# Kernel optimization log

Measured on AMD Instinct MI355X. Metric: run time of the kernel, lower is better.

The kernel has to match this reference:

```python
import jax, jax.numpy as jnp
import numpy as np

B, T, QD, KD, AD = 64, 2048, 512, 512, 512
SCALING = 1.0
NEG = -1e10


def setup_inputs() -> dict:
    key = jax.random.key(0)
    ks = jax.random.split(key, 10)
    s = 0.02
    return {
        "query": jax.random.normal(ks[0], (B, QD), jnp.float32),
        "keys": jax.random.normal(ks[1], (B, T, KD), jnp.float32),
        "value": jax.random.normal(ks[2], (B, T, KD), jnp.float32),
        "cover": jax.random.uniform(ks[3], (B, T), jnp.float32),
        "key_len": jax.random.randint(ks[4], (B,), T // 2, T + 1),
        "Wq": jax.random.normal(ks[5], (QD, AD), jnp.float32) * s,
        "bq": jnp.zeros((AD,), jnp.float32),
        "Wk": jax.random.normal(ks[6], (KD, AD), jnp.float32) * s,
        "Wc": jax.random.normal(ks[7], (1, AD), jnp.float32) * s,
        "Wo": jax.random.normal(ks[8], (AD, 1), jnp.float32) * s,
    }


def reference(query, keys, value, cover, key_len, Wq, bq, Wk, Wc, Wo):
    # projections
    q = query @ Wq + bq                      # [B, A]
    k = jnp.einsum("btd,da->bta", keys, Wk)  # [B, T, A]
    c = cover[..., None] * Wc[0]             # [B, T, A]  (Linear(1, A), no bias)
    # additive energy
    e = jnp.tanh(q[:, None, :] + k + c)      # [B, T, A]
    energy = jnp.einsum("bta,ao->bot", e, Wo)  # [B, 1, T]
    # mask padded positions (t >= key_len)
    mask = jnp.arange(T)[None, None, :] >= key_len[:, None, None]  # [B, 1, T]
    energy = jnp.where(mask, NEG, energy)
    attn = jax.nn.softmax(energy * SCALING, axis=2)  # [B, 1, T]
    context = jnp.einsum("bqt,btd->bqd", attn, value)[:, 0, :]  # [B, KD]
    return context, attn
```

## Files before the change

kernel.cpp:

```cpp
#include <hip/hip_runtime.h>

#define B_ 64
#define T_ 2048
#define D_ 512
#define A_ 512
#define BM 128
#define BK 32
#define NSTEP (D_/BK)

typedef float f32x4_t __attribute__((ext_vector_type(4)));
typedef short bf16x8_t __attribute__((ext_vector_type(8)));

#define GLL16(g, l) __builtin_amdgcn_global_load_lds( \
    (const __attribute__((address_space(1))) void*)(g), \
    (__attribute__((address_space(3))) void*)(l), 16, 0, 0)

__device__ __forceinline__ unsigned int f2bf(float x) {
  union { float f; unsigned int u; } v; v.f = x;
  unsigned int r = ((v.u >> 16) & 1u) + 0x7FFFu;
  return (v.u + r) >> 16;
}
__device__ __forceinline__ unsigned int pack2(float lo, float hi) {
  return (f2bf(lo) & 0xFFFFu) | ((f2bf(hi) & 0xFFFFu) << 16);
}

__global__ void __launch_bounds__(256) qproj_kernel(
    const float* __restrict__ query, const float* __restrict__ Wq,
    const float* __restrict__ bq, float* __restrict__ qbuf) {
  __shared__ float qs[D_];
  const int b = blockIdx.x, tid = threadIdx.x;
  qs[tid] = query[b*D_ + tid];
  qs[tid+256] = query[b*D_ + tid + 256];
  __syncthreads();
  float a0 = bq[tid], a1 = bq[tid+256];
  for (int d = 0; d < D_; ++d) {
    const float qv = qs[d];
    a0 += qv * Wq[d*A_ + tid];
    a1 += qv * Wq[d*A_ + tid + 256];
  }
  qbuf[b*A_ + tid] = a0;
  qbuf[b*A_ + tid+256] = a1;
}

__global__ void __launch_bounds__(256) wkprep_kernel(
    const float* __restrict__ Wk, unsigned int* __restrict__ slab) {
  __shared__ float tile[32][65];
  const int kb = blockIdx.x >> 3;
  const int a0 = (blockIdx.x & 7) * 64;
  const int tid = threadIdx.x;
  for (int p = 0; p < 8; ++p) {
    const int idx = p*256 + tid;
    const int k = idx >> 6, al = idx & 63;
    tile[k][al] = Wk[(kb*32 + k)*A_ + a0 + al];
  }
  __syncthreads();
  const int al = tid >> 2, c = tid & 3;
  const int a = a0 + al;
  uint4 w;
  w.x = pack2(tile[c*8+0][al], tile[c*8+1][al]);
  w.y = pack2(tile[c*8+2][al], tile[c*8+3][al]);
  w.z = pack2(tile[c*8+4][al], tile[c*8+5][al]);
  w.w = pack2(tile[c*8+6][al], tile[c*8+7][al]);
  const int cpos = c ^ ((a >> 1) & 3);
  *(uint4*)(slab + (kb*512 + a)*16 + cpos*4) = w;
}

__global__ void __launch_bounds__(512) energy_kernel(
    const float* __restrict__ keys, const float* __restrict__ cover,
    const int* __restrict__ key_len, const unsigned char* __restrict__ slab,
    const float* __restrict__ qbuf, const float* __restrict__ Wc,
    const float* __restrict__ Wo, float* __restrict__ energy) {
  __shared__ __align__(16) unsigned char Abuf[2][BM*64];
  __shared__ __align__(16) unsigned char Bbuf[2][A_*64];
  __shared__ float redbuf[8][64];

  const int b = blockIdx.y;
  const int t0 = blockIdx.x * BM;
  const int kl = key_len[b];
  if (t0 >= kl) return;

  const int tid = threadIdx.x;
  const int wid = tid >> 6;
  const int lane = tid & 63;
  const int lq = lane >> 4, lr = lane & 15;
  const int wm = wid >> 2, wn = wid & 3;

  const int ar = tid >> 2, ac = tid & 3;
  const float* aptr = keys + ((size_t)b * T_ + t0 + ar) * D_ + ac * 8;
  const int a_dst = ar * 64 + ((ac ^ ((ar >> 1) & 3)) << 4);

  f32x4_t acc[4][8];
  #pragma unroll
  for (int i = 0; i < 4; ++i)
    #pragma unroll
    for (int j = 0; j < 8; ++j) acc[i][j] = 0.0f;

  int a_off[4], b_off[8];
  #pragma unroll
  for (int mf = 0; mf < 4; ++mf) {
    const int r = wm*64 + mf*16 + lr;
    a_off[mf] = r*64 + ((lq ^ ((r >> 1) & 3)) << 4);
  }
  #pragma unroll
  for (int nf = 0; nf < 8; ++nf) {
    const int r = wn*128 + nf*16 + lr;
    b_off[nf] = r*64 + ((lq ^ ((r >> 1) & 3)) << 4);
  }

  {
    const float4 v0 = *(const float4*)(aptr);
    const float4 v1 = *(const float4*)(aptr + 4);
    uint4 w;
    w.x = pack2(v0.x, v0.y); w.y = pack2(v0.z, v0.w);
    w.z = pack2(v1.x, v1.y); w.w = pack2(v1.z, v1.w);
    *(uint4*)(&Abuf[0][a_dst]) = w;
    const unsigned char* g = slab + wid*4096 + lane*16;
    unsigned char* l = &Bbuf[0][wid*4096];
    GLL16(g, l); GLL16(g+1024, l+1024); GLL16(g+2048, l+2048); GLL16(g+3072, l+3072);
  }
  __syncthreads();

  for (int ks = 0; ks < NSTEP; ++ks) {
    const int cur = ks & 1;
    const bool pre = (ks + 1 < NSTEP);
    float4 v0, v1;
    if (pre) {
      const float* p = aptr + (ks + 1) * BK;
      v0 = *(const float4*)(p);
      v1 = *(const float4*)(p + 4);
      const unsigned char* g = slab + (size_t)(ks+1)*32768 + wid*4096 + lane*16;
      unsigned char* l = &Bbuf[cur^1][wid*4096];
      GLL16(g, l); GLL16(g+1024, l+1024); GLL16(g+2048, l+2048); GLL16(g+3072, l+3072);
    }
    bf16x8_t aF[4], bF[8];
    #pragma unroll
    for (int mf = 0; mf < 4; ++mf) aF[mf] = *(const bf16x8_t*)(&Abuf[cur][a_off[mf]]);
    #pragma unroll
    for (int nf = 0; nf < 8; ++nf) bF[nf] = *(const bf16x8_t*)(&Bbuf[cur][b_off[nf]]);
    #pragma unroll
    for (int mf = 0; mf < 4; ++mf)
      #pragma unroll
      for (int nf = 0; nf < 8; ++nf)
        acc[mf][nf] = __builtin_amdgcn_mfma_f32_16x16x32_bf16(aF[mf], bF[nf], acc[mf][nf], 0, 0, 0);
    if (pre) {
      uint4 w;
      w.x = pack2(v0.x, v0.y); w.y = pack2(v0.z, v0.w);
      w.z = pack2(v1.x, v1.y); w.w = pack2(v1.z, v1.w);
      *(uint4*)(&Abuf[cur^1][a_dst]) = w;
    }
    __syncthreads();
  }

  float cov[4][4];
  #pragma unroll
  for (int mf = 0; mf < 4; ++mf)
    #pragma unroll
    for (int j = 0; j < 4; ++j)
      cov[mf][j] = cover[(size_t)b*T_ + t0 + wm*64 + mf*16 + lq*4 + j];

  float ep[4][4];
  #pragma unroll
  for (int mf = 0; mf < 4; ++mf)
    #pragma unroll
    for (int j = 0; j < 4; ++j) ep[mf][j] = 0.f;

  #pragma unroll
  for (int nf = 0; nf < 8; ++nf) {
    const int n = wn*128 + nf*16 + lr;
    const float qv = qbuf[b*A_ + n];
    const float wc = Wc[n];
    const float wo = Wo[n];
    #pragma unroll
    for (int mf = 0; mf < 4; ++mf)
      #pragma unroll
      for (int j = 0; j < 4; ++j) {
        float p = acc[mf][nf][j] + qv + cov[mf][j] * wc;
        p = fminf(fmaxf(p, -15.f), 15.f);
        const float t2 = __expf(2.f * p);
        ep[mf][j] += wo * ((t2 - 1.f) / (t2 + 1.f));
      }
  }
  #pragma unroll
  for (int mf = 0; mf < 4; ++mf)
    #pragma unroll
    for (int j = 0; j < 4; ++j) {
      float v = ep[mf][j];
      v += __shfl_xor(v, 1); v += __shfl_xor(v, 2);
      v += __shfl_xor(v, 4); v += __shfl_xor(v, 8);
      ep[mf][j] = v;
    }
  if (lr == 0) {
    #pragma unroll
    for (int mf = 0; mf < 4; ++mf)
      #pragma unroll
      for (int j = 0; j < 4; ++j)
        redbuf[wid][mf*16 + lq*4 + j] = ep[mf][j];
  }
  __syncthreads();
  if (tid < BM) {
    const int wmm = tid >> 6, rl = tid & 63;
    const float e = redbuf[wmm*4+0][rl] + redbuf[wmm*4+1][rl]
                  + redbuf[wmm*4+2][rl] + redbuf[wmm*4+3][rl];
    energy[b*T_ + t0 + tid] = e;
  }
}

__global__ void __launch_bounds__(1024) softmax_kernel(
    const float* __restrict__ energy, const int* __restrict__ key_len,
    float* __restrict__ attn) {
  __shared__ float sredM[16];
  __shared__ float sredS[16];
  const int b = blockIdx.x, tid = threadIdx.x;
  const int kl = key_len[b];
  const float e0 = (tid < kl) ? energy[b*T_ + tid] : -3.0e38f;
  const float e1 = (tid + 1024 < kl) ? energy[b*T_ + tid + 1024] : -3.0e38f;
  float m = fmaxf(e0, e1);
  for (int s = 32; s; s >>= 1) m = fmaxf(m, __shfl_xor(m, s));
  if ((tid & 63) == 0) sredM[tid >> 6] = m;
  __syncthreads();
  float M = -3.0e38f;
  #pragma unroll
  for (int i = 0; i < 16; ++i) M = fmaxf(M, sredM[i]);
  const float p0 = (tid < kl) ? __expf(e0 - M) : 0.f;
  const float p1 = (tid + 1024 < kl) ? __expf(e1 - M) : 0.f;
  float s = p0 + p1;
  for (int k = 32; k; k >>= 1) s += __shfl_xor(s, k);
  if ((tid & 63) == 0) sredS[tid >> 6] = s;
  __syncthreads();
  float S = 0.f;
  #pragma unroll
  for (int i = 0; i < 16; ++i) S += sredS[i];
  const float inv = 1.f / S;
  attn[b*T_ + tid] = p0 * inv;
  attn[b*T_ + tid + 1024] = p1 * inv;
}

__global__ void __launch_bounds__(256) ctxpart_kernel(
    const float* __restrict__ value, const float* __restrict__ attn,
    const int* __restrict__ key_len, float* __restrict__ partial) {
  __shared__ float att_s[256];
  const int b = blockIdx.y, ch = blockIdx.x;
  const int tid = threadIdx.x;
  const int kl = key_len[b];
  const int tstart = ch * 256;
  const int tend = min(256, kl - tstart);
  float ax = 0.f, ay = 0.f;
  if (tend > 0) {
    att_s[tid] = attn[b*T_ + tstart + tid];
    __syncthreads();
    const float2* vp = (const float2*)(value + ((size_t)b*T_ + tstart)*D_) + tid;
    #pragma unroll 4
    for (int i = 0; i < tend; ++i) {
      const float w = att_s[i];
      const float2 v = vp[(size_t)i * 256];
      ax += w * v.x; ay += w * v.y;
    }
  }
  float2* pp = (float2*)(partial + (size_t)(b*8 + ch)*D_) + tid;
  *pp = make_float2(ax, ay);
}

__global__ void __launch_bounds__(256) ctxsum_kernel(
    const float* __restrict__ partial, float* __restrict__ ctx) {
  const int b = blockIdx.x, tid = threadIdx.x;
  float sx = 0.f, sy = 0.f;
  #pragma unroll
  for (int c = 0; c < 8; ++c) {
    const float2 v = *((const float2*)(partial + (size_t)(b*8 + c)*D_) + tid);
    sx += v.x; sy += v.y;
  }
  *((float2*)(ctx + (size_t)b*D_) + tid) = make_float2(sx, sy);
}

extern "C" void kernel_launch(void* const* d_in, const int* in_sizes, int n_in,
                              void* d_out, int out_size, void* d_ws, size_t ws_size,
                              hipStream_t stream) {
  const float* query  = (const float*)d_in[0];
  const float* keys   = (const float*)d_in[1];
  const float* value  = (const float*)d_in[2];
  const float* cover  = (const float*)d_in[3];
  const int*   key_len= (const int*)d_in[4];
  const float* Wq     = (const float*)d_in[5];
  const float* bq     = (const float*)d_in[6];
  const float* Wk     = (const float*)d_in[7];
  const float* Wc     = (const float*)d_in[8];
  const float* Wo     = (const float*)d_in[9];

  float* out = (float*)d_out;
  float* ctx_out  = out;
  float* attn_out = out + B_*A_;

  float* ws = (float*)d_ws;
  float* qbuf    = ws;
  float* energy  = ws + 32768;
  float* partial = ws + 32768 + 131072;
  unsigned int* slab = (unsigned int*)(ws + 32768 + 131072 + 262144);

  qproj_kernel<<<B_, 256, 0, stream>>>(query, Wq, bq, qbuf);
  wkprep_kernel<<<128, 256, 0, stream>>>(Wk, slab);
  energy_kernel<<<dim3(T_/BM, B_), 512, 0, stream>>>(
      keys, cover, key_len, (const unsigned char*)slab, qbuf, Wc, Wo, energy);
  softmax_kernel<<<B_, 1024, 0, stream>>>(energy, key_len, attn_out);
  ctxpart_kernel<<<dim3(8, B_), 256, 0, stream>>>(value, attn_out, key_len, partial);
  ctxsum_kernel<<<B_, 256, 0, stream>>>(partial, ctx_out);
}
```

Before: 236.8 us.

## Load MFMA fragments straight from global memory, dropping the LDS double buffer

The energy GEMM no longer stages keys and the bf16 Wk slab through swizzled LDS double buffers with per-step barriers. Each wave now loads its own fragments directly from global memory and converts keys to bf16 with the HIP intrinsics. Launch bounds now request 2 blocks per SM, and the slab prep drops its swizzle. This removes LDS traffic and syncs but adds redundant global and L2 reads: each key row is re-read by 4 waves, each slab row by 2 waves. The loads also have no explicit prefetch, so latency hiding relies on occupancy.

```diff
diff --git a/kernel.cpp b/kernel.cpp
--- a/kernel.cpp
+++ b/kernel.cpp
@@ -1,4 +1,5 @@
 #include <hip/hip_runtime.h>
+#include <hip/hip_bf16.h>
 
 #define B_ 64
 #define T_ 2048
@@ -11,17 +12,13 @@
 typedef float f32x4_t __attribute__((ext_vector_type(4)));
 typedef short bf16x8_t __attribute__((ext_vector_type(8)));
 
-#define GLL16(g, l) __builtin_amdgcn_global_load_lds( \
-    (const __attribute__((address_space(1))) void*)(g), \
-    (__attribute__((address_space(3))) void*)(l), 16, 0, 0)
-
-__device__ __forceinline__ unsigned int f2bf(float x) {
-  union { float f; unsigned int u; } v; v.f = x;
-  unsigned int r = ((v.u >> 16) & 1u) + 0x7FFFu;
-  return (v.u + r) >> 16;
-}
-__device__ __forceinline__ unsigned int pack2(float lo, float hi) {
-  return (f2bf(lo) & 0xFFFFu) | ((f2bf(hi) & 0xFFFFu) << 16);
+__device__ __forceinline__ bf16x8_t pack8(float4 v0, float4 v1) {
+  union { __hip_bfloat162 h[4]; bf16x8_t v; } r;
+  r.h[0] = __float22bfloat162_rn(make_float2(v0.x, v0.y));
+  r.h[1] = __float22bfloat162_rn(make_float2(v0.z, v0.w));
+  r.h[2] = __float22bfloat162_rn(make_float2(v1.x, v1.y));
+  r.h[3] = __float22bfloat162_rn(make_float2(v1.z, v1.w));
+  return r.v;
 }
 
 __global__ void __launch_bounds__(256) qproj_kernel(
@@ -56,22 +53,20 @@
   __syncthreads();
   const int al = tid >> 2, c = tid & 3;
   const int a = a0 + al;
-  uint4 w;
-  w.x = pack2(tile[c*8+0][al], tile[c*8+1][al]);
-  w.y = pack2(tile[c*8+2][al], tile[c*8+3][al]);
-  w.z = pack2(tile[c*8+4][al], tile[c*8+5][al]);
-  w.w = pack2(tile[c*8+6][al], tile[c*8+7][al]);
-  const int cpos = c ^ ((a >> 1) & 3);
-  *(uint4*)(slab + (kb*512 + a)*16 + cpos*4) = w;
-}
-
-__global__ void __launch_bounds__(512) energy_kernel(
+  union { __hip_bfloat162 h[2]; uint2 u; } w0, w1;
+  w0.h[0] = __float22bfloat162_rn(make_float2(tile[c*8+0][al], tile[c*8+1][al]));
+  w0.h[1] = __float22bfloat162_rn(make_float2(tile[c*8+2][al], tile[c*8+3][al]));
+  w1.h[0] = __float22bfloat162_rn(make_float2(tile[c*8+4][al], tile[c*8+5][al]));
+  w1.h[1] = __float22bfloat162_rn(make_float2(tile[c*8+6][al], tile[c*8+7][al]));
+  uint4 w = make_uint4(w0.u.x, w0.u.y, w1.u.x, w1.u.y);
+  *(uint4*)(slab + (kb*512 + a)*16 + c*4) = w;
+}
+
+__global__ void __launch_bounds__(512, 2) energy_kernel(
     const float* __restrict__ keys, const float* __restrict__ cover,
     const int* __restrict__ key_len, const unsigned char* __restrict__ slab,
     const float* __restrict__ qbuf, const float* __restrict__ Wc,
     const float* __restrict__ Wo, float* __restrict__ energy) {
-  __shared__ __align__(16) unsigned char Abuf[2][BM*64];
-  __shared__ __align__(16) unsigned char Bbuf[2][A_*64];
   __shared__ float redbuf[8][64];
 
   const int b = blockIdx.y;
@@ -85,9 +80,8 @@
   const int lq = lane >> 4, lr = lane & 15;
   const int wm = wid >> 2, wn = wid & 3;
 
-  const int ar = tid >> 2, ac = tid & 3;
-  const float* aptr = keys + ((size_t)b * T_ + t0 + ar) * D_ + ac * 8;
-  const int a_dst = ar * 64 + ((ac ^ ((ar >> 1) & 3)) << 4);
+  const float* akeys = keys + ((size_t)b * T_ + t0 + wm*64 + lr) * D_ + lq*8;
+  const unsigned char* bslab = slab + (size_t)(wn*128 + lr)*64 + lq*16;
 
   f32x4_t acc[4][8];
   #pragma unroll
@@ -95,60 +89,22 @@
     #pragma unroll
     for (int j = 0; j < 8; ++j) acc[i][j] = 0.0f;
 
-  int a_off[4], b_off[8];
-  #pragma unroll
-  for (int mf = 0; mf < 4; ++mf) {
-    const int r = wm*64 + mf*16 + lr;
-    a_off[mf] = r*64 + ((lq ^ ((r >> 1) & 3)) << 4);
-  }
-  #pragma unroll
-  for (int nf = 0; nf < 8; ++nf) {
-    const int r = wn*128 + nf*16 + lr;
-    b_off[nf] = r*64 + ((lq ^ ((r >> 1) & 3)) << 4);
-  }
-
-  {
-    const float4 v0 = *(const float4*)(aptr);
-    const float4 v1 = *(const float4*)(aptr + 4);
-    uint4 w;
-    w.x = pack2(v0.x, v0.y); w.y = pack2(v0.z, v0.w);
-    w.z = pack2(v1.x, v1.y); w.w = pack2(v1.z, v1.w);
-    *(uint4*)(&Abuf[0][a_dst]) = w;
-    const unsigned char* g = slab + wid*4096 + lane*16;
-    unsigned char* l = &Bbuf[0][wid*4096];
-    GLL16(g, l); GLL16(g+1024, l+1024); GLL16(g+2048, l+2048); GLL16(g+3072, l+3072);
-  }
-  __syncthreads();
-
+  #pragma unroll 2
   for (int ks = 0; ks < NSTEP; ++ks) {
-    const int cur = ks & 1;
-    const bool pre = (ks + 1 < NSTEP);
-    float4 v0, v1;
-    if (pre) {
-      const float* p = aptr + (ks + 1) * BK;
-      v0 = *(const float4*)(p);
-      v1 = *(const float4*)(p + 4);
-      const unsigned char* g = slab + (size_t)(ks+1)*32768 + wid*4096 + lane*16;
-      unsigned char* l = &Bbuf[cur^1][wid*4096];
-      GLL16(g, l); GLL16(g+1024, l+1024); GLL16(g+2048, l+2048); GLL16(g+3072, l+3072);
+    bf16x8_t aF[4], bF[8];
+    #pragma unroll
+    for (int mf = 0; mf < 4; ++mf) {
+      const float* p = akeys + mf*16*D_ + ks*BK;
+      aF[mf] = pack8(*(const float4*)p, *(const float4*)(p + 4));
     }
-    bf16x8_t aF[4], bF[8];
-    #pragma unroll
-    for (int mf = 0; mf < 4; ++mf) aF[mf] = *(const bf16x8_t*)(&Abuf[cur][a_off[mf]]);
-    #pragma unroll
-    for (int nf = 0; nf < 8; ++nf) bF[nf] = *(const bf16x8_t*)(&Bbuf[cur][b_off[nf]]);
+    #pragma unroll
+    for (int nf = 0; nf < 8; ++nf)
+      bF[nf] = *(const bf16x8_t*)(bslab + (size_t)ks*32768 + nf*1024);
     #pragma unroll
     for (int mf = 0; mf < 4; ++mf)
       #pragma unroll
       for (int nf = 0; nf < 8; ++nf)
         acc[mf][nf] = __builtin_amdgcn_mfma_f32_16x16x32_bf16(aF[mf], bF[nf], acc[mf][nf], 0, 0, 0);
-    if (pre) {
-      uint4 w;
-      w.x = pack2(v0.x, v0.y); w.y = pack2(v0.z, v0.w);
-      w.z = pack2(v1.x, v1.y); w.w = pack2(v1.z, v1.w);
-      *(uint4*)(&Abuf[cur^1][a_dst]) = w;
-    }
-    __syncthreads();
   }
 
   float cov[4][4];
```

Result: slower. 321.8 us (+35.9%).
